# Performance work log

Measured on AMD Instinct MI355X. Metric: run time of the kernel, lower is better.

## Reference

```python
import jax, jax.numpy as jnp
import numpy as np

D_MODEL = 1024
N_HEADS = 16
HEAD_DIM = D_MODEL // N_HEADS


def setup_inputs() -> dict:
    key = jax.random.key(0)
    ks = jax.random.split(key, 9)
    B, L = 2, 2048
    s = 1.0 / np.sqrt(D_MODEL)
    return {
        "x": jax.random.normal(ks[0], (B, L, D_MODEL), dtype=jnp.float32),
        "q_w": jax.random.normal(ks[1], (D_MODEL, D_MODEL), dtype=jnp.float32) * s,
        "q_b": jnp.zeros((D_MODEL,), dtype=jnp.float32),
        "k_w": jax.random.normal(ks[2], (D_MODEL, D_MODEL), dtype=jnp.float32) * s,
        "k_b": jnp.zeros((D_MODEL,), dtype=jnp.float32),
        "v_w": jax.random.normal(ks[3], (D_MODEL, D_MODEL), dtype=jnp.float32) * s,
        "v_b": jnp.zeros((D_MODEL,), dtype=jnp.float32),
        "o_w": jax.random.normal(ks[4], (D_MODEL, D_MODEL), dtype=jnp.float32) * s,
        "o_b": jnp.zeros((D_MODEL,), dtype=jnp.float32),
    }


def _rope_tables(L, dtype):
    # inv_freq: [head_dim//2]
    inv_freq = 1.0 / (10000.0 ** (jnp.arange(0, HEAD_DIM, 2, dtype=dtype) / HEAD_DIM))
    t = jnp.arange(L, dtype=dtype)
    freqs = t[:, None] * inv_freq[None, :]          # [L, hd/2]
    emb = jnp.concatenate([freqs, freqs], axis=-1)  # [L, hd]
    return jnp.cos(emb), jnp.sin(emb)


def _rotate_half(x):
    x1, x2 = x[..., : HEAD_DIM // 2], x[..., HEAD_DIM // 2 :]
    return jnp.concatenate([-x2, x1], axis=-1)


def reference(x, q_w, q_b, k_w, k_b, v_w, v_b, o_w, o_b):
    B, L, D = x.shape
    H, hd = N_HEADS, HEAD_DIM
    # Linear (torch: x @ W.T + b), then split heads -> [B, H, L, hd]
    def proj(w, b):
        y = jnp.einsum("bld,ed->ble", x, w) + b
        return y.reshape(B, L, H, hd).transpose(0, 2, 1, 3)

    q, k, v = proj(q_w, q_b), proj(k_w, k_b), proj(v_w, v_b)

    cos, sin = _rope_tables(L, x.dtype)  # [L, hd] each, broadcast over B,H
    q = q * cos + _rotate_half(q) * sin
    k = k * cos + _rotate_half(k) * sin

    scores = jnp.einsum("bhqd,bhkd->bhqk", q, k) / jnp.sqrt(jnp.asarray(hd, x.dtype))
    attn = jax.nn.softmax(scores, axis=-1)
    out = jnp.einsum("bhqk,bhkd->bhqd", attn, v)
    out = out.transpose(0, 2, 1, 3).reshape(B, L, D)
    return jnp.einsum("bld,ed->ble", out, o_w) + o_b
```

## Files before the change

kernel.cpp:

```cpp
#include <hip/hip_runtime.h>
#include <math.h>

#define SEQ   2048
#define NH    16
#define HD    64
#define DM    1024
#define BATCH 2
#define MROWS (BATCH*SEQ)

typedef __attribute__((ext_vector_type(8))) short short8;
typedef __attribute__((ext_vector_type(4))) float f32x4;
typedef __attribute__((ext_vector_type(16))) float f32x16;
typedef unsigned short ushort;
typedef unsigned int uint;

__device__ __forceinline__ ushort f2bf(float x){
  unsigned int u = __float_as_uint(x);
  unsigned int r = (u + 0x7fffu + ((u>>16)&1u)) >> 16;
  return (ushort)r;
}
__device__ __forceinline__ void gload16(const ushort* g, ushort* l){
  __builtin_amdgcn_global_load_lds(
      (const __attribute__((address_space(1))) unsigned int*)(g),
      (__attribute__((address_space(3))) unsigned int*)(l), 16, 0, 0);
}

__global__ void rope_tables_kernel(float* __restrict__ cosT, float* __restrict__ sinT){
  int idx = blockIdx.x*blockDim.x + threadIdx.x;
  if (idx >= SEQ*32) return;
  int i = idx & 31, l = idx >> 5;
  float e = (float)(2*i) / 64.0f;
  float inv = 1.0f / powf(10000.0f, e);
  float ang = (float)l * inv;
  cosT[idx] = cosf(ang);
  sinT[idx] = sinf(ang);
}

__global__ void cast_all_kernel(
    const float* __restrict__ X,
    const float* __restrict__ wq, const float* __restrict__ wk,
    const float* __restrict__ wv, const float* __restrict__ wo,
    ushort* __restrict__ Xh,
    ushort* __restrict__ hq, ushort* __restrict__ hk,
    ushort* __restrict__ hv, ushort* __restrict__ ho)
{
  int idx = blockIdx.x*blockDim.x + threadIdx.x;
  const float* src; ushort* dh; int off;
  const int NX = (MROWS*DM) >> 2;
  if (idx < NX){ src = X; dh = Xh; off = idx; }
  else {
    int t = idx - NX;
    int sel = t >> 18;
    off = t & 262143;
    src = sel==0 ? wq : sel==1 ? wk : sel==2 ? wv : wo;
    dh  = sel==0 ? hq : sel==1 ? hk : sel==2 ? hv : ho;
  }
  float4 v = ((const float4*)src)[off];
  uint2 hp;
  hp.x = (unsigned)f2bf(v.x) | ((unsigned)f2bf(v.y)<<16);
  hp.y = (unsigned)f2bf(v.z) | ((unsigned)f2bf(v.w)<<16);
  ((uint2*)dh)[off] = hp;
}

__global__ __launch_bounds__(256) void gemm_qkv_mfma(
    const ushort* __restrict__ Xh,
    const ushort* __restrict__ Whq, const ushort* __restrict__ Whk, const ushort* __restrict__ Whv,
    const float* __restrict__ bq, const float* __restrict__ bk, const float* __restrict__ bv,
    const float* __restrict__ cosT, const float* __restrict__ sinT,
    ushort* __restrict__ Qb, ushort* __restrict__ Kb, ushort* __restrict__ Vb)
{
  __shared__ __align__(16) ushort As[128*64];
  __shared__ __align__(16) ushort Bs[128*64];
  const int tid = threadIdx.x, w = tid>>6, lane = tid&63;
  const int c = lane & 15, g = lane >> 4;
  const int wr = w >> 1, wc = w & 1;
  const int m0   = blockIdx.x * 128;
  const int ncat = blockIdx.y * 128;
  const int which = ncat >> 10;
  const int n0    = ncat & 1023;
  const ushort* Bhi = which==0 ? Whq : which==1 ? Whk : Whv;
  const float*  bias= which==0 ? bq  : which==1 ? bk  : bv;

  const int srow = lane >> 3;
  const int scol = ((lane & 7) ^ srow) << 3;

  f32x4 acc[4][4] = {};
  for (int k0 = 0; k0 < DM; k0 += 64){
    __syncthreads();
    #pragma unroll
    for (int i=0;i<4;i++){
      const int rb = w*32 + i*8;
      gload16(Xh  + (size_t)(m0 + rb + srow)*DM + k0 + scol, &As[rb*64]);
      gload16(Bhi + (size_t)(n0 + rb + srow)*DM + k0 + scol, &Bs[rb*64]);
    }
    __syncthreads();
    #pragma unroll
    for (int kc=0;kc<2;kc++){
      short8 a[4], b[4];
      #pragma unroll
      for (int m=0;m<4;m++){
        int row = wr*64 + m*16 + c;
        a[m] = *(const short8*)&As[row*64 + ((((kc<<2)+g) ^ (row&7))<<3)];
      }
      #pragma unroll
      for (int n=0;n<4;n++){
        int row = wc*64 + n*16 + c;
        b[n] = *(const short8*)&Bs[row*64 + ((((kc<<2)+g) ^ (row&7))<<3)];
      }
      #pragma unroll
      for (int m=0;m<4;m++)
        #pragma unroll
        for (int n=0;n<4;n++)
          acc[m][n] = __builtin_amdgcn_mfma_f32_16x16x32_bf16(a[m], b[n], acc[m][n], 0,0,0);
    }
  }

  const int hh = (n0 + wc*64) >> 6;
  ushort* Out = which==0 ? Qb : which==1 ? Kb : Vb;
  #pragma unroll
  for (int m=0;m<4;m++){
    #pragma unroll
    for (int r=0;r<4;r++){
      int mrow = m0 + wr*64 + m*16 + 4*g + r;
      int bb = mrow >> 11, l = mrow & (SEQ-1);
      size_t obase = (((size_t)bb*NH + hh)*SEQ + l)*HD;
      size_t vbase = (((size_t)bb*NH + hh)*HD)*SEQ + l;
      #pragma unroll
      for (int n=0;n<2;n++){
        int d1 = n*16 + c, d2 = d1 + 32;
        float v1 = acc[m][n  ][r] + bias[hh*64 + d1];
        float v2 = acc[m][n+2][r] + bias[hh*64 + d2];
        if (which < 2){
          float co = cosT[l*32 + d1], si = sinT[l*32 + d1];
          float o1 = v1*co - v2*si;
          float o2 = v2*co + v1*si;
          if (which == 0){ o1 *= 0.125f; o2 *= 0.125f; }
          Out[obase + d1] = f2bf(o1);
          Out[obase + d2] = f2bf(o2);
        } else {
          Out[vbase + (size_t)d1*SEQ] = f2bf(v1);
          Out[vbase + (size_t)d2*SEQ] = f2bf(v2);
        }
      }
    }
  }
}

__global__ __launch_bounds__(256) void flash_mfma_kernel(
    const ushort* __restrict__ Qb, const ushort* __restrict__ Kb,
    const ushort* __restrict__ VTg, ushort* __restrict__ AOh)
{
  __shared__ __align__(16) ushort Ks[2][8][512];
  __shared__ __align__(16) ushort Vs[2][8][512];

  const int tid  = threadIdx.x;
  const int w    = tid >> 6;
  const int lane = tid & 63;
  const int c    = lane & 31;
  const int h    = lane >> 5;

  const int hw = blockIdx.x;
  const int lg = (hw & 7)*64 + (hw >> 3);
  const int bx = lg & 15, hd = (lg >> 4) & 15, b = lg >> 8;
  const int bh = b*NH + hd;
  const int q0 = bx*128 + w*32;

  const ushort* Kbase = Kb  + (size_t)bh*SEQ*HD;
  const ushort* Vbase = VTg + (size_t)bh*HD*SEQ;

  const ushort* Qrow = Qb + ((size_t)bh*SEQ + q0 + c)*HD + 8*h;
  short8 qf[4];
  #pragma unroll
  for (int kc=0;kc<4;kc++) qf[kc] = *(const short8*)(Qrow + kc*16);

  short8 ones;
  #pragma unroll
  for (int i=0;i<8;i++) ones[i] = (short)0x3F80;

  f32x16 oacc[2] = {};
  f32x16 sacc = {};

  #define STAGE(bf, t0) { \
    _Pragma("unroll") for (int i_=0;i_<2;i_++){ \
      int n_ = 2*w + i_; \
      gload16(Kbase + (size_t)((t0) + (n_>>2)*32 + c)*HD + (n_&3)*16 + 8*h, &Ks[bf][n_][0]); \
      gload16(Vbase + (size_t)((n_>>2)*32 + c)*SEQ + (t0) + ((n_>>1)&1)*32 + (n_&1)*16 + 8*h, &Vs[bf][n_][0]); \
    } }

  STAGE(0, 0)
  __syncthreads();

  int buf = 0;
  for (int t0 = 0; t0 < SEQ; t0 += 64){
    if (t0 + 64 < SEQ){
      STAGE(buf ^ 1, t0 + 64)
    }

    #pragma unroll
    for (int kb=0; kb<2; kb++){
      f32x16 s = {};
      __builtin_amdgcn_s_setprio(1);
      #pragma unroll
      for (int kc=0;kc<4;kc++){
        short8 kf = *(const short8*)&Ks[buf][kb*4+kc][lane*8];
        s = __builtin_amdgcn_mfma_f32_32x32x16_bf16(kf, qf[kc], s, 0,0,0);
      }
      __builtin_amdgcn_s_setprio(0);

      uint pk[8];
      #pragma unroll
      for (int i=0;i<8;i++){
        float p0 = __expf(s[2*i]);
        float p1 = __expf(s[2*i+1]);
        asm("v_cvt_pk_bf16_f32 %0, %1, %2" : "=v"(pk[i]) : "v"(p0), "v"(p1));
      }
      asm volatile("v_permlane32_swap_b32 %0, %1" : "+v"(pk[0]), "+v"(pk[2]));
      asm volatile("v_permlane32_swap_b32 %0, %1" : "+v"(pk[1]), "+v"(pk[3]));
      asm volatile("v_permlane32_swap_b32 %0, %1" : "+v"(pk[4]), "+v"(pk[6]));
      asm volatile("v_permlane32_swap_b32 %0, %1" : "+v"(pk[5]), "+v"(pk[7]));
      short8 pa0, pa1;
      ((uint*)&pa0)[0]=pk[0]; ((uint*)&pa0)[1]=pk[1]; ((uint*)&pa0)[2]=pk[2]; ((uint*)&pa0)[3]=pk[3];
      ((uint*)&pa1)[0]=pk[4]; ((uint*)&pa1)[1]=pk[5]; ((uint*)&pa1)[2]=pk[6]; ((uint*)&pa1)[3]=pk[7];

      __builtin_amdgcn_s_setprio(1);
      #pragma unroll
      for (int db=0; db<2; db++){
        short8 v0 = *(const short8*)&Vs[buf][db*4 + kb*2 + 0][lane*8];
        short8 v1 = *(const short8*)&Vs[buf][db*4 + kb*2 + 1][lane*8];
        oacc[db] = __builtin_amdgcn_mfma_f32_32x32x16_bf16(pa0, v0, oacc[db], 0,0,0);
        oacc[db] = __builtin_amdgcn_mfma_f32_32x32x16_bf16(pa1, v1, oacc[db], 0,0,0);
      }
      sacc = __builtin_amdgcn_mfma_f32_32x32x16_bf16(pa0, ones, sacc, 0,0,0);
      sacc = __builtin_amdgcn_mfma_f32_32x32x16_bf16(pa1, ones, sacc, 0,0,0);
      __builtin_amdgcn_s_setprio(0);
    }

    __syncthreads();
    buf ^= 1;
  }
  #undef STAGE

  float inv[16];
  #pragma unroll
  for (int r=0;r<16;r++) inv[r] = 1.0f / sacc[r];
  #pragma unroll
  for (int db=0; db<2; db++){
    #pragma unroll
    for (int r=0;r<16;r++){
      int q = q0 + (r&3) + 8*(r>>2) + 4*h;
      AOh[((size_t)b*SEQ + q)*DM + hd*HD + db*32 + c] = f2bf(oacc[db][r] * inv[r]);
    }
  }
}

__global__ __launch_bounds__(256) void gemm_o_mfma(
    const ushort* __restrict__ AOh, const ushort* __restrict__ Who,
    const float* __restrict__ bo, float* __restrict__ Y)
{
  __shared__ __align__(16) ushort As[128*64];
  __shared__ __align__(16) ushort Bs[128*64];
  const int tid = threadIdx.x, w = tid>>6, lane = tid&63;
  const int c = lane & 15, g = lane >> 4;
  const int wr = w >> 1, wc = w & 1;
  const int m0 = blockIdx.x * 128;
  const int n0 = blockIdx.y * 128;

  const int srow = lane >> 3;
  const int scol = ((lane & 7) ^ srow) << 3;

  f32x4 acc[4][4] = {};
  for (int k0 = 0; k0 < DM; k0 += 64){
    __syncthreads();
    #pragma unroll
    for (int i=0;i<4;i++){
      const int rb = w*32 + i*8;
      gload16(AOh + (size_t)(m0 + rb + srow)*DM + k0 + scol, &As[rb*64]);
      gload16(Who + (size_t)(n0 + rb + srow)*DM + k0 + scol, &Bs[rb*64]);
    }
    __syncthreads();
    #pragma unroll
    for (int kc=0;kc<2;kc++){
      short8 a[4], b[4];
      #pragma unroll
      for (int m=0;m<4;m++){
        int row = wr*64 + m*16 + c;
        a[m] = *(const short8*)&As[row*64 + ((((kc<<2)+g) ^ (row&7))<<3)];
      }
      #pragma unroll
      for (int n=0;n<4;n++){
        int row = wc*64 + n*16 + c;
        b[n] = *(const short8*)&Bs[row*64 + ((((kc<<2)+g) ^ (row&7))<<3)];
      }
      #pragma unroll
      for (int m=0;m<4;m++)
        #pragma unroll
        for (int n=0;n<4;n++)
          acc[m][n] = __builtin_amdgcn_mfma_f32_16x16x32_bf16(a[m], b[n], acc[m][n], 0,0,0);
    }
  }

  #pragma unroll
  for (int m=0;m<4;m++){
    #pragma unroll
    for (int r=0;r<4;r++){
      int mrow = m0 + wr*64 + m*16 + 4*g + r;
      #pragma unroll
      for (int n=0;n<4;n++){
        int ncol = n0 + wc*64 + n*16 + c;
        Y[(size_t)mrow*DM + ncol] = acc[m][n][r] + bo[ncol];
      }
    }
  }
}

extern "C" void kernel_launch(void* const* d_in, const int* in_sizes, int n_in,
                              void* d_out, int out_size, void* d_ws, size_t ws_size,
                              hipStream_t stream)
{
  const float* x  = (const float*)d_in[0];
  const float* qw = (const float*)d_in[1];
  const float* qb = (const float*)d_in[2];
  const float* kw = (const float*)d_in[3];
  const float* kb = (const float*)d_in[4];
  const float* vw = (const float*)d_in[5];
  const float* vb = (const float*)d_in[6];
  const float* ow = (const float*)d_in[7];
  const float* ob = (const float*)d_in[8];
  float* out = (float*)d_out;

  const size_t NE = (size_t)MROWS*DM;
  const size_t WE = (size_t)DM*DM;
  float* cosT = (float*)d_ws;
  float* sinT = cosT + SEQ*32;
  ushort* p = (ushort*)(sinT + SEQ*32);
  ushort* Xh  = p;            p += NE;
  ushort* Whq = p;            p += WE;
  ushort* Whk = p;            p += WE;
  ushort* Whv = p;            p += WE;
  ushort* Who = p;            p += WE;
  ushort* Qb  = p;            p += NE;
  ushort* Kb  = p;            p += NE;
  ushort* Vb  = p;            p += NE;
  ushort* AOh = p;            p += NE;

  hipLaunchKernelGGL(rope_tables_kernel, dim3((SEQ*32+255)/256), dim3(256), 0, stream, cosT, sinT);
  hipLaunchKernelGGL(cast_all_kernel, dim3((NE/4 + WE)/256), dim3(256), 0, stream,
                     x, qw, kw, vw, ow, Xh, Whq, Whk, Whv, Who);
  hipLaunchKernelGGL(gemm_qkv_mfma, dim3(MROWS/128, 3072/128), dim3(256), 0, stream,
                     Xh, Whq, Whk, Whv, qb, kb, vb, cosT, sinT, Qb, Kb, Vb);
  hipLaunchKernelGGL(flash_mfma_kernel, dim3(512), dim3(256), 0, stream,
                     Qb, Kb, Vb, AOh);
  hipLaunchKernelGGL(gemm_o_mfma, dim3(MROWS/128, DM/128), dim3(256), 0, stream,
                     AOh, Who, ob, out);
}
```

Before: 139.1 us.

## Store K and V in pre-tiled LDS-image layout so flash loads are contiguous

The QKV projection epilogue now writes K and V into a blocked layout that matches the shared-memory tile image used by the attention kernel, replacing the row-major K and the transposed V. The flash kernel's staging loads become fully contiguous 16-byte-per-lane chunks instead of strided gathers. In exchange, the projection's scattered 2-byte stores are more complex and less coalesced, and the layout couples the two kernels tightly.

```diff
diff --git a/kernel.cpp b/kernel.cpp
--- a/kernel.cpp
+++ b/kernel.cpp
@@ -124,7 +124,8 @@
       int mrow = m0 + wr*64 + m*16 + 4*g + r;
       int bb = mrow >> 11, l = mrow & (SEQ-1);
       size_t obase = (((size_t)bb*NH + hh)*SEQ + l)*HD;
-      size_t vbase = (((size_t)bb*NH + hh)*HD)*SEQ + l;
+      size_t tbase = (((size_t)bb*NH + hh)*(SEQ/64) + (l>>6))*4096;
+      const int kbl = (l>>5)&1;
       #pragma unroll
       for (int n=0;n<2;n++){
         int d1 = n*16 + c, d2 = d1 + 32;
@@ -134,12 +135,22 @@
           float co = cosT[l*32 + d1], si = sinT[l*32 + d1];
           float o1 = v1*co - v2*si;
           float o2 = v2*co + v1*si;
-          if (which == 0){ o1 *= 0.125f; o2 *= 0.125f; }
-          Out[obase + d1] = f2bf(o1);
-          Out[obase + d2] = f2bf(o2);
+          if (which == 0){
+            Out[obase + d1] = f2bf(o1*0.125f);
+            Out[obase + d2] = f2bf(o2*0.125f);
+          } else {
+            size_t k1 = tbase + (size_t)((kbl*4 + (d1>>4))*512 + ((l&31) + 32*((d1>>3)&1))*8 + (d1&7));
+            size_t k2 = tbase + (size_t)((kbl*4 + (d2>>4))*512 + ((l&31) + 32*((d2>>3)&1))*8 + (d2&7));
+            Out[k1] = f2bf(o1);
+            Out[k2] = f2bf(o2);
+          }
         } else {
-          Out[vbase + (size_t)d1*SEQ] = f2bf(v1);
-          Out[vbase + (size_t)d2*SEQ] = f2bf(v2);
+          const int lpos = ((l&31) + 32*((l>>3)&1))*8 + (l&7);
+          size_t v1o = tbase + (size_t)(((d1>>5)*4 + kbl*2 + ((l>>4)&1))*512 + ((d1&31) + 32*((l>>3)&1))*8 + (l&7));
+          size_t v2o = tbase + (size_t)(((d2>>5)*4 + kbl*2 + ((l>>4)&1))*512 + ((d2&31) + 32*((l>>3)&1))*8 + (l&7));
+          (void)lpos;
+          Out[v1o] = f2bf(v1);
+          Out[v2o] = f2bf(v2);
         }
       }
     }
@@ -148,7 +159,7 @@
 
 __global__ __launch_bounds__(256) void flash_mfma_kernel(
     const ushort* __restrict__ Qb, const ushort* __restrict__ Kb,
-    const ushort* __restrict__ VTg, ushort* __restrict__ AOh)
+    const ushort* __restrict__ Vb, ushort* __restrict__ AOh)
 {
   __shared__ __align__(16) ushort Ks[2][8][512];
   __shared__ __align__(16) ushort Vs[2][8][512];
@@ -165,8 +176,8 @@
   const int bh = b*NH + hd;
   const int q0 = bx*128 + w*32;
 
-  const ushort* Kbase = Kb  + (size_t)bh*SEQ*HD;
-  const ushort* Vbase = VTg + (size_t)bh*HD*SEQ;
+  const ushort* Kimg = Kb + (size_t)bh*SEQ*HD;
+  const ushort* Vimg = Vb + (size_t)bh*SEQ*HD;
 
   const ushort* Qrow = Qb + ((size_t)bh*SEQ + q0 + c)*HD + 8*h;
   short8 qf[4];
@@ -183,8 +194,8 @@
   #define STAGE(bf, t0) { \
     _Pragma("unroll") for (int i_=0;i_<2;i_++){ \
       int n_ = 2*w + i_; \
-      gload16(Kbase + (size_t)((t0) + (n_>>2)*32 + c)*HD + (n_&3)*16 + 8*h, &Ks[bf][n_][0]); \
-      gload16(Vbase + (size_t)((n_>>2)*32 + c)*SEQ + (t0) + ((n_>>1)&1)*32 + (n_&1)*16 + 8*h, &Vs[bf][n_][0]); \
+      gload16(Kimg + ((t0)>>6)*4096 + n_*512 + lane*8, &Ks[bf][n_][0]); \
+      gload16(Vimg + ((t0)>>6)*4096 + n_*512 + lane*8, &Vs[bf][n_][0]); \
     } }
 
   STAGE(0, 0)
```

New measurement: 143.7 us. +3.3%, slower.
